# Kernel tuning notes

Hardware: AMD Instinct MI355X
Metric: run time of the kernel (lower is better)

The kernel has to match this reference:

```python
import jax, jax.numpy as jnp
import numpy as np

B, S, H = 2, 8192, 1024
NUM_HEADS = 16
HEAD_DIM = H // NUM_HEADS
KERNEL = 7
DILATION = 1
SCALE = 1.0 / np.sqrt(HEAD_DIM)


def setup_inputs() -> dict:
    key = jax.random.key(0)
    ks = jax.random.split(key, 9)
    init = 0.02
    return {
        "hidden_states": jax.random.normal(ks[0], (B, S, H), dtype=jnp.float32),
        "w_q": jax.random.normal(ks[1], (H, H), dtype=jnp.float32) * init,
        "b_q": jnp.zeros((H,), dtype=jnp.float32),
        "w_k": jax.random.normal(ks[2], (H, H), dtype=jnp.float32) * init,
        "b_k": jnp.zeros((H,), dtype=jnp.float32),
        "w_v": jax.random.normal(ks[3], (H, H), dtype=jnp.float32) * init,
        "b_v": jnp.zeros((H,), dtype=jnp.float32),
        "w_o": jax.random.normal(ks[4], (H, H), dtype=jnp.float32) * init,
        "b_o": jnp.zeros((H,), dtype=jnp.float32),
    }


def reference(hidden_states, w_q, b_q, w_k, b_k, w_v, b_v, w_o, b_o):
    b, s, h = hidden_states.shape
    # QKV projections (weights stored [in, out])
    q = hidden_states @ w_q + b_q
    k = hidden_states @ w_k + b_k
    v = hidden_states @ w_v + b_v
    # [B, nH, S, hd]
    q = q.reshape(b, s, NUM_HEADS, HEAD_DIM).transpose(0, 2, 1, 3)
    k = k.reshape(b, s, NUM_HEADS, HEAD_DIM).transpose(0, 2, 1, 3)
    v = v.reshape(b, s, NUM_HEADS, HEAD_DIM).transpose(0, 2, 1, 3)

    # Neighborhood window indices: for query i, keys at i + (j - K//2)*dilation
    offsets = (jnp.arange(KERNEL) - KERNEL // 2) * DILATION  # [K]
    idx = jnp.arange(s)[:, None] + offsets[None, :]          # [S, K]
    valid = (idx >= 0) & (idx < s)                           # [S, K]
    idx_c = jnp.clip(idx, 0, s - 1)

    k_win = k[:, :, idx_c, :]  # [B, nH, S, K, hd]
    v_win = v[:, :, idx_c, :]  # [B, nH, S, K, hd]

    scores = jnp.einsum('bhsd,bhskd->bhsk', q, k_win) * SCALE
    scores = jnp.where(valid[None, None], scores, -jnp.inf)
    attn = jax.nn.softmax(scores, axis=-1)                   # [B, nH, S, K]
    out = jnp.einsum('bhsk,bhskd->bhsd', attn, v_win)        # [B, nH, S, hd]

    out = out.transpose(0, 2, 1, 3).reshape(b, s, h)
    return out @ w_o + b_o
```

## Files before the change

### kernel.cpp

```cpp
#include <hip/hip_runtime.h>


typedef __bf16 bf16x8 __attribute__((ext_vector_type(8)));
typedef float f32x4 __attribute__((ext_vector_type(4)));
typedef int int4v __attribute__((ext_vector_type(4)));
typedef __attribute__((address_space(1))) void as1_void;
typedef __attribute__((address_space(3))) void as3_void;

__device__ __forceinline__ float bf2f(unsigned short u) {
    union { unsigned int u; float f; } c;
    c.u = ((unsigned int)u) << 16;
    return c.f;
}
__device__ __forceinline__ unsigned short f2bf(float f) {
    union { float f; unsigned int u; } c;
    c.f = f;
    unsigned int u = c.u;
    u += 0x7fffu + ((u >> 16) & 1u);
    return (unsigned short)(u >> 16);
}

__global__ __launch_bounds__(256) void prep(
    const float* __restrict__ X, const float* __restrict__ w0,
    const float* __restrict__ w1, const float* __restrict__ w2,
    const float* __restrict__ w3, const float* __restrict__ bq,
    const float* __restrict__ bk, const float* __restrict__ bv,
    unsigned short* __restrict__ Xb, unsigned short* __restrict__ t0,
    unsigned short* __restrict__ t3, float* __restrict__ biasQ) {
    __shared__ unsigned short tile[32][33];
    const int bid = blockIdx.x;
    if (bid < 16384) {
        int i = bid * 256 + threadIdx.x;
        float4 v = ((const float4*)X)[i];
        ushort4 o;
        o.x = f2bf(v.x); o.y = f2bf(v.y); o.z = f2bf(v.z); o.w = f2bf(v.w);
        ((ushort4*)Xb)[i] = o;
    } else if (bid < 20480) {
        const int t = bid - 16384;
        const int z = t >> 10;
        const int rem = t & 1023;
        const float* W = (z == 0) ? w0 : (z == 1) ? w1 : (z == 2) ? w2 : w3;
        unsigned short* Wt = (z == 3) ? t3 : t0 + (size_t)z * 1048576;
        const int c0 = (rem & 31) * 32;
        const int r0 = (rem >> 5) * 32;
        const int tx = threadIdx.x & 31;
        const int ty = threadIdx.x >> 5;
#pragma unroll
        for (int i = 0; i < 32; i += 8)
            tile[ty + i][tx] = f2bf(W[(size_t)(r0 + ty + i) * 1024 + c0 + tx]);
        __syncthreads();
#pragma unroll
        for (int i = 0; i < 32; i += 8)
            Wt[(size_t)(c0 + ty + i) * 1024 + r0 + tx] = tile[tx][ty + i];
    } else {
        int i = (bid - 20480) * 256 + threadIdx.x;
        if (i < 3072)
            biasQ[i] = (i < 1024) ? bq[i] : ((i < 2048) ? bk[i - 1024] : bv[i - 2048]);
    }
}

template <int MODE, int MT>
__device__ __forceinline__ void gemm_body(
    const unsigned short* __restrict__ A, const unsigned short* __restrict__ Bt,
    const float* __restrict__ bias, float* __restrict__ Cf,
    unsigned short* __restrict__ Cb, unsigned short* __restrict__ Vt,
    int N, int K) {
    __shared__ unsigned short smem[MT * 2048 + 8192];
    const int tid = threadIdx.x;
    const int lane = tid & 63;
    const int wave = tid >> 6;
    const int bm = blockIdx.y * (MT * 32);
    const int bn = blockIdx.x * 128;
    const int wm = (wave >> 1) * (MT * 16);
    const int wn = (wave & 1) * 64;
    const int quad = lane >> 4;
    const int mr = lane & 15;

    const unsigned short* gA[MT];
    const unsigned short* gB[4];
    char* lA[MT];
    char* lB[4];
#pragma unroll
    for (int k = 0; k < MT; ++k) {
        const int q = (k * 4 + wave) * 64 + lane;
        const int row = q >> 3;
        const int c8 = (q & 7) ^ (row & 7);
        gA[k] = A + (size_t)(bm + row) * K + c8 * 8;
        lA[k] = (char*)smem + (size_t)(k * 4 + wave) * 1024;
    }
#pragma unroll
    for (int k = 0; k < 4; ++k) {
        const int q = (k * 4 + wave) * 64 + lane;
        const int row = q >> 3;
        const int c8 = (q & 7) ^ (row & 7);
        gB[k] = Bt + (size_t)(bn + row) * K + c8 * 8;
        lB[k] = (char*)smem + (size_t)MT * 4096 + (size_t)(k * 4 + wave) * 1024;
    }

    f32x4 acc[MT][4] = {};

    for (int kt = 0; kt < K; kt += 64) {
#pragma unroll
        for (int k = 0; k < MT; ++k) {
            __builtin_amdgcn_global_load_lds((as1_void*)gA[k], (as3_void*)lA[k], 16, 0, 0);
            gA[k] += 64;
        }
#pragma unroll
        for (int k = 0; k < 4; ++k) {
            __builtin_amdgcn_global_load_lds((as1_void*)gB[k], (as3_void*)lB[k], 16, 0, 0);
            gB[k] += 64;
        }
        __syncthreads();

#pragma unroll
        for (int kk = 0; kk < 2; ++kk) {
            const int c8 = (kk * 4 + quad) ^ (mr & 7);
            bf16x8 af[MT], bfr[4];
#pragma unroll
            for (int i = 0; i < MT; ++i)
                af[i] = *(const bf16x8*)(smem + (wm + i * 16 + mr) * 64 + c8 * 8);
#pragma unroll
            for (int j = 0; j < 4; ++j)
                bfr[j] = *(const bf16x8*)(smem + MT * 2048 + (wn + j * 16 + mr) * 64 + c8 * 8);
#pragma unroll
            for (int i = 0; i < MT; ++i)
#pragma unroll
                for (int j = 0; j < 4; ++j)
                    acc[i][j] = __builtin_amdgcn_mfma_f32_16x16x32_bf16(
                        af[i], bfr[j], acc[i][j], 0, 0, 0);
        }
        __syncthreads();
    }

    if (MODE == 0) {
        float* epf = (float*)smem + wave * 1280;
#pragma unroll
        for (int j = 0; j < 4; ++j) {
            const int gcol0 = bn + wn + j * 16;
            const float bv = bias[gcol0 + mr];
#pragma unroll
            for (int h2 = 0; h2 < MT / 4; ++h2) {
#pragma unroll
                for (int i2 = 0; i2 < 4; ++i2)
#pragma unroll
                    for (int r = 0; r < 4; ++r)
                        epf[(i2 * 16 + quad * 4 + r) * 20 + mr] = acc[h2 * 4 + i2][j][r] + bv;
#pragma unroll
                for (int p = 0; p < 4; ++p) {
                    const int dr = p * 16 + (lane >> 2);
                    const int ch = lane & 3;
                    f32x4 v = *(const f32x4*)(epf + dr * 20 + ch * 4);
                    *(f32x4*)(Cf + (size_t)(bm + wm + h2 * 64 + dr) * N + gcol0 + ch * 4) = v;
                }
            }
        }
    } else if (bn < 2048) {
        unsigned short* ep = smem + wave * 4096;
#pragma unroll
        for (int j = 0; j < 4; ++j) {
            const int gcol0 = bn + wn + j * 16;
            const float bv = bias[gcol0 + mr];
#pragma unroll
            for (int i = 0; i < MT; ++i)
#pragma unroll
                for (int r = 0; r < 4; ++r)
                    ep[(i * 16 + quad * 4 + r) * 20 + mr] = f2bf(acc[i][j][r] + bv);
#pragma unroll
            for (int p = 0; p < MT / 2; ++p) {
                const int dr = p * 32 + (lane >> 1);
                const int ch = lane & 1;
                int4v v = *(const int4v*)(ep + dr * 20 + ch * 8);
                *(int4v*)(Cb + (size_t)(bm + wm + dr) * 2048 + gcol0 + ch * 8) = v;
            }
        }
    } else {
        unsigned short* ep = smem + wave * 4096;
        const int bb = (bm + wm) >> 13;
        const int ssb = (bm + wm) & 8191;
#pragma unroll
        for (int j = 0; j < 4; ++j) {
            const int gcol = bn + wn + j * 16 + mr;
            const float bv = bias[gcol];
#pragma unroll
            for (int i = 0; i < MT; ++i)
#pragma unroll
                for (int r = 0; r < 4; ++r)
                    ep[mr * 132 + i * 16 + quad * 4 + r] = f2bf(acc[i][j][r] + bv);
            const size_t vrow0 = (size_t)(bb * 1024 + (bn - 2048) + wn + j * 16);
#pragma unroll
            for (int p = 0; p < 4; ++p) {
                const int dr = p * 4 + (lane >> 4);
                const int ch = lane & 15;
                int4v v = *(const int4v*)(ep + dr * 132 + ch * 8);
                *(int4v*)(Vt + (vrow0 + dr) * 8192 + ssb + ch * 8) = v;
            }
        }
    }
}

__global__ __launch_bounds__(256, 2) void gemm_qkv(
    const unsigned short* __restrict__ A, const unsigned short* __restrict__ Bt,
    const float* __restrict__ bias, unsigned short* __restrict__ Cb,
    unsigned short* __restrict__ Vt, int N, int K) {
    gemm_body<1, 8>(A, Bt, bias, nullptr, Cb, Vt, N, K);
}

__global__ __launch_bounds__(256, 4) void gemm_out(
    const unsigned short* __restrict__ A, const unsigned short* __restrict__ Bt,
    const float* __restrict__ bias, float* __restrict__ Cf, int N, int K) {
    gemm_body<0, 4>(A, Bt, bias, Cf, nullptr, nullptr, N, K);
}

__global__ __launch_bounds__(256) void attn_mfma(
    const unsigned short* __restrict__ QK, const unsigned short* __restrict__ Vt,
    unsigned short* __restrict__ out) {
    __shared__ unsigned short sP[4][64 * 104];
    const int tid = threadIdx.x;
    const int lane = tid & 63;
    const int wave = tid >> 6;
    const int quad = lane >> 4;
    const int cc = lane & 15;
    const int w = blockIdx.x * 4 + wave;
    const int b = w >> 11;
    const int h = (w >> 7) & 15;
    const int st = w & 127;
    const int s0 = st << 6;
    const int win0 = s0 - 8;
    const size_t tokBase = (size_t)b * 8192;
    unsigned short* P = sP[wave];

    {
        int4v z = {0, 0, 0, 0};
#pragma unroll
        for (int i = 0; i < 13; ++i)
            *(int4v*)(P + i * 512 + lane * 8) = z;
    }

    f32x4 accS[4][5] = {};
#pragma unroll
    for (int kc = 0; kc < 2; ++kc) {
        bf16x8 qf[4], kf[5];
#pragma unroll
        for (int mt = 0; mt < 4; ++mt)
            qf[mt] = *(const bf16x8*)(QK + (tokBase + s0 + mt * 16 + cc) * 2048
                                      + h * 64 + kc * 32 + quad * 8);
#pragma unroll
        for (int nt = 0; nt < 5; ++nt) {
            int row = win0 + nt * 16 + cc;
            row = row < 0 ? 0 : (row > 8191 ? 8191 : row);
            kf[nt] = *(const bf16x8*)(QK + (tokBase + row) * 2048
                                      + 1024 + h * 64 + kc * 32 + quad * 8);
        }
#pragma unroll
        for (int mt = 0; mt < 4; ++mt)
#pragma unroll
            for (int nt = 0; nt < 5; ++nt)
                accS[mt][nt] = __builtin_amdgcn_mfma_f32_16x16x32_bf16(
                    qf[mt], kf[nt], accS[mt][nt], 0, 0, 0);
    }

    const float NEG = -__builtin_inff();
#pragma unroll
    for (int mt = 0; mt < 4; ++mt) {
#pragma unroll
        for (int r = 0; r < 4; ++r) {
            const int mrow = mt * 16 + quad * 4 + r;
            float v[5];
#pragma unroll
            for (int nt = 0; nt < 5; ++nt) {
                const int k = nt * 16 + cc;
                const int rel = k - mrow;
                const int sidx = win0 + k;
                const bool ok = (rel >= 5) & (rel <= 11) & (sidx >= 0) & (sidx < 8192);
                v[nt] = ok ? accS[mt][nt][r] * 0.125f : NEG;
            }
            float mx = v[0];
#pragma unroll
            for (int nt = 1; nt < 5; ++nt) mx = fmaxf(mx, v[nt]);
#pragma unroll
            for (int off = 8; off >= 1; off >>= 1) mx = fmaxf(mx, __shfl_xor(mx, off));
            float p[5], sum = 0.f;
#pragma unroll
            for (int nt = 0; nt < 5; ++nt) {
                p[nt] = __builtin_amdgcn_exp2f((v[nt] - mx) * 1.44269504f);
                sum += p[nt];
            }
#pragma unroll
            for (int off = 8; off >= 1; off >>= 1) sum += __shfl_xor(sum, off);
            const float inv = __builtin_amdgcn_rcpf(sum);
#pragma unroll
            for (int nt = 0; nt < 5; ++nt)
                P[mrow * 104 + nt * 16 + cc] = f2bf(p[nt] * inv);
        }
    }

    f32x4 accO[4][4] = {};
#pragma unroll
    for (int kc = 0; kc < 3; ++kc) {
        bf16x8 pf[4], vf[4];
#pragma unroll
        for (int mt = 0; mt < 4; ++mt)
            pf[mt] = *(const bf16x8*)(P + (mt * 16 + cc) * 104 + kc * 32 + quad * 8);
        {
            int pos = win0 + kc * 32 + quad * 8;
            pos = pos < 0 ? 0 : (pos > 8184 ? 8184 : pos);
#pragma unroll
            for (int nt = 0; nt < 4; ++nt)
                vf[nt] = *(const bf16x8*)(Vt + ((size_t)(b * 16 + h) * 64 + nt * 16 + cc) * 8192 + pos);
        }
#pragma unroll
        for (int mt = 0; mt < 4; ++mt)
#pragma unroll
            for (int nt = 0; nt < 4; ++nt)
                accO[mt][nt] = __builtin_amdgcn_mfma_f32_16x16x32_bf16(
                    pf[mt], vf[nt], accO[mt][nt], 0, 0, 0);
    }

#pragma unroll
    for (int mt = 0; mt < 4; ++mt)
#pragma unroll
        for (int nt = 0; nt < 4; ++nt)
#pragma unroll
            for (int r = 0; r < 4; ++r)
                P[(mt * 16 + quad * 4 + r) * 72 + nt * 16 + cc] = f2bf(accO[mt][nt][r]);

#pragma unroll
    for (int pass = 0; pass < 8; ++pass) {
        const int row = pass * 8 + (lane >> 3);
        const int ch = lane & 7;
        int4v vv = *(const int4v*)(P + row * 72 + ch * 8);
        *(int4v*)(out + (tokBase + s0 + row) * 1024 + h * 64 + ch * 8) = vv;
    }
}

extern "C" void kernel_launch(void* const* d_in, const int* in_sizes, int n_in,
                              void* d_out, int out_size, void* d_ws, size_t ws_size,
                              hipStream_t stream) {
    (void)in_sizes; (void)n_in; (void)out_size; (void)ws_size;
    const float* X  = (const float*)d_in[0];
    const float* wq = (const float*)d_in[1];
    const float* bq = (const float*)d_in[2];
    const float* wk = (const float*)d_in[3];
    const float* bk = (const float*)d_in[4];
    const float* wv = (const float*)d_in[5];
    const float* bv = (const float*)d_in[6];
    const float* wo = (const float*)d_in[7];
    const float* bo = (const float*)d_in[8];
    float* out = (float*)d_out;

    char* ws = (char*)d_ws;
    unsigned short* Xb    = (unsigned short*)(ws);
    unsigned short* WtQKV = (unsigned short*)(ws + 33554432);
    unsigned short* WtO   = (unsigned short*)(ws + 39845888);
    unsigned short* QK    = (unsigned short*)(ws + 41943040);
    unsigned short* Vt    = (unsigned short*)(ws + 109051904);
    unsigned short* AttnO = (unsigned short*)(ws + 142606336);
    float*          biasQ = (float*)(ws + 176160768);

    prep<<<20492, 256, 0, stream>>>(X, wq, wk, wv, wo, bq, bk, bv,
                                    Xb, WtQKV, WtO, biasQ);

    gemm_qkv<<<dim3(24, 64), 256, 0, stream>>>(Xb, WtQKV, biasQ, QK, Vt, 3072, 1024);

    attn_mfma<<<1024, 256, 0, stream>>>(QK, Vt, AttnO);

    gemm_out<<<dim3(8, 128), 256, 0, stream>>>(AttnO, WtO, bo, out, 1024, 1024);
}
```

Baseline: 336.3 us.

## Replace QKV GEMM with 256x256-tile 8-wave pipelined kernel using direct-to-LDS loads

Replaces the generic QKV projection GEMM with a dedicated 512-thread kernel that computes 256x256 output tiles. It double-buffers A and B in LDS using global_load_lds with XOR swizzling, interleaves four staged loads with four MFMA phases per k-step, raises wave priority during MFMA, and swizzles block order for L2 locality. The aim is to overlap global loads with matrix math and raise arithmetic intensity per block. The cost is heavy LDS use (128KB), many barriers and a larger register footprint.

```diff
diff --git a/kernel.cpp b/kernel.cpp
--- a/kernel.cpp
+++ b/kernel.cpp
@@ -59,6 +59,194 @@
     }
 }
 
+__global__ __launch_bounds__(512, 2) void gemm_qkv8(
+    const unsigned short* __restrict__ A, const unsigned short* __restrict__ Bt,
+    const float* __restrict__ bias, unsigned short* __restrict__ Cb,
+    unsigned short* __restrict__ Vt) {
+    constexpr int K = 1024;
+    constexpr int NT = 16;
+    __shared__ unsigned short smem[65536];
+    const int tid  = threadIdx.x;
+    const int lane = tid & 63;
+    const int wave = tid >> 6;
+    const int quad = lane >> 4;
+    const int mr   = lane & 15;
+
+    const int id  = blockIdx.x;
+    const int swz = (id & 7) * 96 + (id >> 3);
+    const int bm  = (swz / 12) * 256;
+    const int bn  = (swz % 12) * 256;
+    const int wm  = (wave >> 2) * 128;
+    const int wn  = (wave & 3) * 64;
+
+    const int r0 = tid >> 3;
+    const int g8 = ((lane & 7) ^ ((lane >> 3) & 7)) * 8;
+    const unsigned short* srcA = A  + (size_t)(bm + r0) * K + g8;
+    const unsigned short* srcB = Bt + (size_t)(bn + r0) * K + g8;
+
+    auto stage = [&](const unsigned short* gb, int ldsByte, int kt) {
+#pragma unroll
+        for (int l = 0; l < 2; ++l)
+            __builtin_amdgcn_global_load_lds(
+                (const as1_void*)(gb + (size_t)l * 65536 + kt),
+                (as3_void*)((char*)smem + ldsByte + l * 8192 + tid * 16),
+                16, 0, 0);
+    };
+
+    stage(srcA,          0,     0);
+    stage(srcA + 131072, 16384, 0);
+    stage(srcB,          32768, 0);
+    stage(srcB + 131072, 49152, 0);
+    stage(srcB,          65536 + 32768, 64);
+    stage(srcB + 131072, 65536 + 49152, 64);
+    asm volatile("s_waitcnt vmcnt(4)" ::: "memory");
+    asm volatile("s_barrier" ::: "memory");
+
+    const int aRow = (wm + mr) * 64;
+    const int bRow = 16384 + (wn + mr) * 64;
+    const int c8_0 = ((0 * 4 + quad) ^ (mr & 7)) * 8;
+    const int c8_1 = ((1 * 4 + quad) ^ (mr & 7)) * 8;
+
+    f32x4 acc[8][4] = {};
+    bf16x8 af[4][2], b01[2][2], b23[2][2];
+
+    for (int t = 0; t < NT; ++t) {
+        const int bufS  = (t & 1) << 15;
+        const int nbufB = ((t + 1) & 1) << 16;
+        const int cbufB = (t & 1) << 16;
+        const int ktA = (t + 1 < NT ? t + 1 : NT - 1) * 64;
+        const int ktB = (t + 2 < NT ? t + 2 : NT - 1) * 64;
+
+#pragma unroll
+        for (int i = 0; i < 4; ++i) {
+            af[i][0] = *(const bf16x8*)(smem + bufS + aRow + i * 1024 + c8_0);
+            af[i][1] = *(const bf16x8*)(smem + bufS + aRow + i * 1024 + c8_1);
+        }
+#pragma unroll
+        for (int j = 0; j < 2; ++j) {
+            b01[j][0] = *(const bf16x8*)(smem + bufS + bRow + j * 1024 + c8_0);
+            b01[j][1] = *(const bf16x8*)(smem + bufS + bRow + j * 1024 + c8_1);
+        }
+        stage(srcA, nbufB, ktA);
+        asm volatile("s_barrier" ::: "memory");
+        asm volatile("s_waitcnt lgkmcnt(0)" ::: "memory");
+        __builtin_amdgcn_s_setprio(1);
+#pragma unroll
+        for (int i = 0; i < 4; ++i)
+#pragma unroll
+            for (int j = 0; j < 2; ++j) {
+                acc[i][j] = __builtin_amdgcn_mfma_f32_16x16x32_bf16(af[i][0], b01[j][0], acc[i][j], 0, 0, 0);
+                acc[i][j] = __builtin_amdgcn_mfma_f32_16x16x32_bf16(af[i][1], b01[j][1], acc[i][j], 0, 0, 0);
+            }
+        __builtin_amdgcn_s_setprio(0);
+        asm volatile("s_barrier" ::: "memory");
+
+#pragma unroll
+        for (int j = 0; j < 2; ++j) {
+            b23[j][0] = *(const bf16x8*)(smem + bufS + bRow + (j + 2) * 1024 + c8_0);
+            b23[j][1] = *(const bf16x8*)(smem + bufS + bRow + (j + 2) * 1024 + c8_1);
+        }
+        stage(srcA + 131072, nbufB + 16384, ktA);
+        asm volatile("s_barrier" ::: "memory");
+        asm volatile("s_waitcnt lgkmcnt(0)" ::: "memory");
+        __builtin_amdgcn_s_setprio(1);
+#pragma unroll
+        for (int i = 0; i < 4; ++i)
+#pragma unroll
+            for (int j = 0; j < 2; ++j) {
+                acc[i][j + 2] = __builtin_amdgcn_mfma_f32_16x16x32_bf16(af[i][0], b23[j][0], acc[i][j + 2], 0, 0, 0);
+                acc[i][j + 2] = __builtin_amdgcn_mfma_f32_16x16x32_bf16(af[i][1], b23[j][1], acc[i][j + 2], 0, 0, 0);
+            }
+        __builtin_amdgcn_s_setprio(0);
+        asm volatile("s_barrier" ::: "memory");
+
+#pragma unroll
+        for (int i = 0; i < 4; ++i) {
+            af[i][0] = *(const bf16x8*)(smem + bufS + aRow + (i + 4) * 1024 + c8_0);
+            af[i][1] = *(const bf16x8*)(smem + bufS + aRow + (i + 4) * 1024 + c8_1);
+        }
+        stage(srcB, cbufB + 32768, ktB);
+        asm volatile("s_barrier" ::: "memory");
+        asm volatile("s_waitcnt lgkmcnt(0)" ::: "memory");
+        __builtin_amdgcn_s_setprio(1);
+#pragma unroll
+        for (int i = 0; i < 4; ++i)
+#pragma unroll
+            for (int j = 0; j < 2; ++j) {
+                acc[i + 4][j + 2] = __builtin_amdgcn_mfma_f32_16x16x32_bf16(af[i][0], b23[j][0], acc[i + 4][j + 2], 0, 0, 0);
+                acc[i + 4][j + 2] = __builtin_amdgcn_mfma_f32_16x16x32_bf16(af[i][1], b23[j][1], acc[i + 4][j + 2], 0, 0, 0);
+            }
+        __builtin_amdgcn_s_setprio(0);
+        asm volatile("s_barrier" ::: "memory");
+
+        stage(srcB + 131072, cbufB + 49152, ktB);
+        asm volatile("s_barrier" ::: "memory");
+        asm volatile("s_waitcnt lgkmcnt(0)" ::: "memory");
+        __builtin_amdgcn_s_setprio(1);
+#pragma unroll
+        for (int i = 0; i < 4; ++i)
+#pragma unroll
+            for (int j = 0; j < 2; ++j) {
+                acc[i + 4][j] = __builtin_amdgcn_mfma_f32_16x16x32_bf16(af[i][0], b01[j][0], acc[i + 4][j], 0, 0, 0);
+                acc[i + 4][j] = __builtin_amdgcn_mfma_f32_16x16x32_bf16(af[i][1], b01[j][1], acc[i + 4][j], 0, 0, 0);
+            }
+        __builtin_amdgcn_s_setprio(0);
+        asm volatile("s_waitcnt vmcnt(4)" ::: "memory");
+        asm volatile("s_barrier" ::: "memory");
+    }
+
+    asm volatile("s_waitcnt vmcnt(0) lgkmcnt(0)" ::: "memory");
+    asm volatile("s_barrier" ::: "memory");
+
+    unsigned short* ep = smem + wave * 8192;
+    if (bn < 2048) {
+#pragma unroll
+        for (int h = 0; h < 2; ++h) {
+#pragma unroll
+            for (int j = 0; j < 4; ++j) {
+                const float bvv = bias[bn + wn + j * 16 + mr];
+#pragma unroll
+                for (int i = 0; i < 4; ++i)
+#pragma unroll
+                    for (int r = 0; r < 4; ++r)
+                        ep[(i * 16 + quad * 4 + r) * 68 + j * 16 + mr] =
+                            f2bf(acc[h * 4 + i][j][r] + bvv);
+            }
+#pragma unroll
+            for (int p = 0; p < 8; ++p) {
+                const int row = p * 8 + (lane >> 3);
+                const int gr = lane & 7;
+                int4v v = *(const int4v*)(ep + row * 68 + gr * 8);
+                *(int4v*)(Cb + (size_t)(bm + wm + h * 64 + row) * 2048 + bn + wn + gr * 8) = v;
+            }
+        }
+    } else {
+        const int bb = (bm + wm) >> 13;
+        const int sb = (bm + wm) & 8191;
+        const size_t vrow0 = (size_t)bb * 8388608 + (size_t)(bn - 2048 + wn) * 8192 + sb;
+#pragma unroll
+        for (int h = 0; h < 2; ++h) {
+#pragma unroll
+            for (int j = 0; j < 4; ++j) {
+                const float bvv = bias[bn + wn + j * 16 + mr];
+#pragma unroll
+                for (int i = 0; i < 4; ++i)
+#pragma unroll
+                    for (int r = 0; r < 4; ++r)
+                        ep[(j * 16 + mr) * 68 + h * 0 + i * 16 + quad * 4 + r] =
+                            f2bf(acc[h * 4 + i][j][r] + bvv);
+            }
+#pragma unroll
+            for (int p = 0; p < 8; ++p) {
+                const int d = p * 8 + (lane >> 3);
+                const int gr = lane & 7;
+                int4v v = *(const int4v*)(ep + d * 68 + gr * 8);
+                *(int4v*)(Vt + vrow0 + (size_t)d * 8192 + h * 64 + gr * 8) = v;
+            }
+        }
+    }
+}
+
 template <int MODE, int MT>
 __device__ __forceinline__ void gemm_body(
     const unsigned short* __restrict__ A, const unsigned short* __restrict__ Bt,
@@ -154,55 +342,7 @@
                 }
             }
         }
-    } else if (bn < 2048) {
-        unsigned short* ep = smem + wave * 4096;
-#pragma unroll
-        for (int j = 0; j < 4; ++j) {
-            const int gcol0 = bn + wn + j * 16;
-            const float bv = bias[gcol0 + mr];
-#pragma unroll
-            for (int i = 0; i < MT; ++i)
-#pragma unroll
-                for (int r = 0; r < 4; ++r)
-                    ep[(i * 16 + quad * 4 + r) * 20 + mr] = f2bf(acc[i][j][r] + bv);
-#pragma unroll
-            for (int p = 0; p < MT / 2; ++p) {
-                const int dr = p * 32 + (lane >> 1);
-                const int ch = lane & 1;
-                int4v v = *(const int4v*)(ep + dr * 20 + ch * 8);
-                *(int4v*)(Cb + (size_t)(bm + wm + dr) * 2048 + gcol0 + ch * 8) = v;
-            }
-        }
-    } else {
-        unsigned short* ep = smem + wave * 4096;
-        const int bb = (bm + wm) >> 13;
-        const int ssb = (bm + wm) & 8191;
-#pragma unroll
-        for (int j = 0; j < 4; ++j) {
-            const int gcol = bn + wn + j * 16 + mr;
-            const float bv = bias[gcol];
-#pragma unroll
-            for (int i = 0; i < MT; ++i)
-#pragma unroll
-                for (int r = 0; r < 4; ++r)
-                    ep[mr * 132 + i * 16 + quad * 4 + r] = f2bf(acc[i][j][r] + bv);
-            const size_t vrow0 = (size_t)(bb * 1024 + (bn - 2048) + wn + j * 16);
-#pragma unroll
-            for (int p = 0; p < 4; ++p) {
-                const int dr = p * 4 + (lane >> 4);
-                const int ch = lane & 15;
-                int4v v = *(const int4v*)(ep + dr * 132 + ch * 8);
-                *(int4v*)(Vt + (vrow0 + dr) * 8192 + ssb + ch * 8) = v;
-            }
-        }
-    }
-}
-
-__global__ __launch_bounds__(256, 2) void gemm_qkv(
-    const unsigned short* __restrict__ A, const unsigned short* __restrict__ Bt,
-    const float* __restrict__ bias, unsigned short* __restrict__ Cb,
-    unsigned short* __restrict__ Vt, int N, int K) {
-    gemm_body<1, 8>(A, Bt, bias, nullptr, Cb, Vt, N, K);
+    }
 }
 
 __global__ __launch_bounds__(256, 4) void gemm_out(
@@ -360,7 +500,7 @@
     prep<<<20492, 256, 0, stream>>>(X, wq, wk, wv, wo, bq, bk, bv,
                                     Xb, WtQKV, WtO, biasQ);
 
-    gemm_qkv<<<dim3(24, 64), 256, 0, stream>>>(Xb, WtQKV, biasQ, QK, Vt, 3072, 1024);
+    gemm_qkv8<<<768, 512, 0, stream>>>(Xb, WtQKV, biasQ, QK, Vt);
 
     attn_mfma<<<1024, 256, 0, stream>>>(QK, Vt, AttnO);
 
```

Measured after the change: 324.2 us. 3.6% less time.
